# Optimization experiments

Hardware: AMD Instinct MI355X
Metric: run time of the kernel (lower is better)

## Reference

```python
import jax, jax.numpy as jnp
import numpy as np

EMBED_DIM = 1024
HEADS = 16
HEAD_DIM = EMBED_DIM // HEADS
N, SEQ = 2, 2048


def setup_inputs() -> dict:
    key = jax.random.key(0)
    ks = jax.random.split(key, 9)
    s = 1.0 / np.sqrt(HEAD_DIM)
    inp = {
        "values": jax.random.normal(ks[0], (N, SEQ, EMBED_DIM), jnp.float32),
        "keys": jax.random.normal(ks[1], (N, SEQ, EMBED_DIM), jnp.float32),
        "query": jax.random.normal(ks[2], (N, SEQ, EMBED_DIM), jnp.float32),
        "mask": jax.random.randint(ks[3], (N, 1, SEQ, SEQ), 0, 2, jnp.int32),
        # per-head projection weights (torch Linear: y = x @ W.T)
        "Wv": jax.random.normal(ks[4], (HEAD_DIM, HEAD_DIM), jnp.float32) * s,
        "Wk": jax.random.normal(ks[5], (HEAD_DIM, HEAD_DIM), jnp.float32) * s,
        "Wq": jax.random.normal(ks[6], (HEAD_DIM, HEAD_DIM), jnp.float32) * s,
        "Wo": jax.random.normal(ks[7], (EMBED_DIM, EMBED_DIM), jnp.float32) * (1.0 / np.sqrt(EMBED_DIM)),
        "bo": jax.random.normal(ks[8], (EMBED_DIM,), jnp.float32) * 0.01,
    }
    return inp


def reference(values, keys, query, mask, Wv, Wk, Wq, Wo, bo):
    n, q_len = query.shape[0], query.shape[1]
    v_len, k_len = values.shape[1], keys.shape[1]
    # reshape to [N, len, H, D]
    v = values.reshape(n, v_len, HEADS, HEAD_DIM)
    k = keys.reshape(n, k_len, HEADS, HEAD_DIM)
    q = query.reshape(n, q_len, HEADS, HEAD_DIM)
    # per-head linear projections (shared weight across heads), torch: x @ W.T
    v = jnp.einsum("nlhd,ed->nlhe", v, Wv)
    k = jnp.einsum("nlhd,ed->nlhe", k, Wk)
    q = jnp.einsum("nlhd,ed->nlhe", q, Wq)
    # energy: [N, H, Q, K]
    energy = jnp.einsum("nqhd,nkhd->nhqk", q, k)
    energy = jnp.where(mask == 0, jnp.float32(-1e20), energy)
    # NOTE: original scales by sqrt(embed_dim), not sqrt(head_dim)
    attention = jax.nn.softmax(energy / jnp.sqrt(jnp.float32(EMBED_DIM)), axis=3)
    out = jnp.einsum("nhql,nlhd->nqhd", attention, v).reshape(n, q_len, EMBED_DIM)
    out = out @ Wo.T + bo  # fc_out; dropout is identity in eval mode
    return out
```

## Files before the change

### kernel.cpp

```cpp
#include <hip/hip_runtime.h>
#include <hip/hip_bf16.h>

#define NB 2
#define SEQ 2048
#define HEADS 16
#define HD 64
#define ED 1024

typedef __bf16 bf16x8 __attribute__((ext_vector_type(8)));
typedef float f32x4 __attribute__((ext_vector_type(4)));
typedef unsigned short u16x8 __attribute__((ext_vector_type(8)));
typedef unsigned short u16x4 __attribute__((ext_vector_type(4)));

__device__ __forceinline__ unsigned short f2bf(float f) {
    unsigned u = __builtin_bit_cast(unsigned, f);
    u += 0x7fffu + ((u >> 16) & 1u);
    return (unsigned short)(u >> 16);
}

__device__ __forceinline__ bf16x8 cvt8(const float* __restrict__ p) {
    const float4* p4 = (const float4*)p;
    float4 a = p4[0], b = p4[1];
    u16x8 u;
    u[0] = f2bf(a.x); u[1] = f2bf(a.y); u[2] = f2bf(a.z); u[3] = f2bf(a.w);
    u[4] = f2bf(b.x); u[5] = f2bf(b.y); u[6] = f2bf(b.z); u[7] = f2bf(b.w);
    return __builtin_bit_cast(bf16x8, u);
}

__device__ __forceinline__ bf16x8 ldfrag(const void* p) {
    uint4 v = *(const uint4*)p;
    return __builtin_bit_cast(bf16x8, v);
}

__device__ __forceinline__ f32x4 mfma16(bf16x8 a, bf16x8 b, f32x4 c) {
    return __builtin_amdgcn_mfma_f32_16x16x32_bf16(a, b, c, 0, 0, 0);
}

__device__ __forceinline__ unsigned packbf(float lo, float hi) {
    unsigned a = __builtin_bit_cast(unsigned, hi) + 0x8000u;
    unsigned b = __builtin_bit_cast(unsigned, lo) + 0x8000u;
    return __builtin_amdgcn_perm(a, b, 0x07060302u);
}

#define GLOAD_LDS(gp, lp) \
    __builtin_amdgcn_global_load_lds( \
        (const __attribute__((address_space(1))) unsigned int*)(gp), \
        (__attribute__((address_space(3))) unsigned int*)(lp), 16, 0, 0)

#define QSCALE 0.04508422f

__global__ __launch_bounds__(256) void mask_bits_kernel(
    const int* __restrict__ mask, unsigned long long* __restrict__ bits)
{
    size_t i = (size_t)blockIdx.x * 256 + threadIdx.x;
    int m = mask[i];
    unsigned long long b = __ballot(m != 0);
    if ((threadIdx.x & 63) == 0) bits[i >> 6] = b;
}

__global__ __launch_bounds__(256) void wo_cvt_kernel(
    const float* __restrict__ Wo, unsigned short* __restrict__ Wob)
{
    size_t i = ((size_t)blockIdx.x * 256 + threadIdx.x) * 4;
    float4 v = *(const float4*)(Wo + i);
    u16x4 u;
    u[0] = f2bf(v.x); u[1] = f2bf(v.y); u[2] = f2bf(v.z); u[3] = f2bf(v.w);
    *(u16x4*)(Wob + i) = u;
}

__global__ __launch_bounds__(256) void proj_kernel(
    const float* __restrict__ qin, const float* __restrict__ kin, const float* __restrict__ vin,
    const float* __restrict__ Wq, const float* __restrict__ Wk, const float* __restrict__ Wv,
    unsigned short* __restrict__ Qb, unsigned short* __restrict__ Kb,
    unsigned short* __restrict__ Vt)
{
    __shared__ __align__(16) char tile[64 * 144];

    int t3  = blockIdx.x >> 10;
    int rem = blockIdx.x & 1023;
    int h   = rem >> 6;
    int rt  = rem & 63;
    int wave = threadIdx.x >> 6, lane = threadIdx.x & 63;
    int quad = lane >> 4, l16 = lane & 15;

    const float* in = (t3 == 0) ? qin : ((t3 == 1) ? kin : vin);
    const float* W  = (t3 == 0) ? Wq  : ((t3 == 1) ? Wk  : Wv);

    int r0 = rt * 64 + wave * 16;

    bf16x8 bf0[4], bf1[4];
#pragma unroll
    for (int sl = 0; sl < 4; ++sl) {
        const float* wrow = W + (sl * 16 + l16) * 64;
        bf0[sl] = cvt8(wrow + quad * 8);
        bf1[sl] = cvt8(wrow + 32 + quad * 8);
    }
    const float* xrow = in + (size_t)(r0 + l16) * ED + h * 64;
    bf16x8 af0 = cvt8(xrow + quad * 8);
    bf16x8 af1 = cvt8(xrow + 32 + quad * 8);

    f32x4 acc[4];
#pragma unroll
    for (int sl = 0; sl < 4; ++sl) {
        f32x4 c = {0.f, 0.f, 0.f, 0.f};
        c = mfma16(af0, bf0[sl], c);
        c = mfma16(af1, bf1[sl], c);
        acc[sl] = c;
    }
    float sc = (t3 == 0) ? QSCALE : 1.0f;

    size_t nh = (size_t)((r0 >> 11) * HEADS + h);
    int rl = lane >> 3, cl = lane & 7;

    if (t3 != 2) {
#pragma unroll
        for (int r = 0; r < 4; ++r) {
            int srow = wave * 16 + quad * 4 + r;
#pragma unroll
            for (int sl = 0; sl < 4; ++sl)
                *(unsigned short*)(tile + srow * 144 + (sl * 16 + l16) * 2) =
                    f2bf(acc[sl][r] * sc);
        }
        unsigned short* dst = (t3 == 0) ? Qb : Kb;
        int s0 = (r0 & 2047);
#pragma unroll
        for (int g = 0; g < 2; ++g) {
            int lrow = wave * 16 + g * 8 + rl;
            uint4 v = *(const uint4*)(tile + lrow * 144 + cl * 16);
            *(uint4*)(dst + (nh * SEQ + (s0 & ~15) + g * 8 + rl) * HD + cl * 8) = v;
        }
    } else {
#pragma unroll
        for (int r = 0; r < 4; ++r) {
            int srow = wave * 16 + quad * 4 + r;
#pragma unroll
            for (int sl = 0; sl < 4; ++sl)
                *(unsigned short*)(tile + (sl * 16 + l16) * 144 + srow * 2) =
                    f2bf(acc[sl][r]);
        }
        __syncthreads();
        int s_tile = rt & 31;
#pragma unroll
        for (int g = 0; g < 2; ++g) {
            int erow = wave * 16 + g * 8 + rl;
            uint4 v = *(const uint4*)(tile + erow * 144 + cl * 16);
            *(uint4*)(Vt + ((nh * 32 + s_tile) * 64 + erow) * 64 + cl * 8) = v;
        }
    }
}

template <int SPLIT>
__global__ __launch_bounds__(256, 4) void attn_kernel(
    const unsigned short* __restrict__ Qb, const unsigned short* __restrict__ Kb,
    const unsigned short* __restrict__ Vt2, const unsigned long long* __restrict__ mb,
    unsigned short* __restrict__ Ab, float* __restrict__ Of, float* __restrict__ Ls)
{
    __shared__ __align__(16) char smem[24576 + 4 * 2304];

    int tid = threadIdx.x;
    int wave = tid >> 6, lane = tid & 63;
    int quad = lane >> 4, l16 = lane & 15;

    int b   = blockIdx.x;
    int xcd = b & 7;
    int j   = b >> 3;
    int nh, qb, half;
    if (SPLIT) { nh = xcd * 4 + (j >> 5); int r = j & 31; qb = r >> 1; half = r & 1; }
    else       { nh = xcd * 4 + (j >> 4); qb = j & 15; half = 0; }
    int n = nh >> 4, h = nh & 15;
    int q0 = qb * 128 + wave * 32;

    size_t headoff = (size_t)nh * SEQ * HD;
    bf16x8 qf[2][2];
#pragma unroll
    for (int t = 0; t < 2; ++t) {
        const unsigned short* qrow = Qb + headoff + (size_t)(q0 + t * 16 + l16) * HD;
        qf[t][0] = ldfrag(qrow + quad * 8);
        qf[t][1] = ldfrag(qrow + 32 + quad * 8);
    }

    int srow = lane >> 3, sslot = lane & 7;
    int stoff = srow * 128 + (((sslot - srow) & 7) * 16);

    int rotA = ((quad + l16) & 7) * 16;
    int aK0 = l16 * 128 + rotA;
    int aV  = 16384 + l16 * 128 + rotA;
    int aVx = aV ^ 64;
    char* pbase = smem + 24576 + wave * 2304;
    char* pw = pbase + l16 * 144 + quad * 8;
    char* pr = pbase + l16 * 144 + quad * 16;

    const unsigned short* gK = Kb + headoff;
    const unsigned short* gV = Vt2 + (size_t)nh * (32 * 4096);
    const unsigned long long* mbase = mb + (size_t)n * (SEQ * SEQ / 64)
                                         + (size_t)(q0 + l16) * (SEQ / 64);

    u16x8 ou;
#pragma unroll
    for (int jj = 0; jj < 8; ++jj) ou[jj] = 0x3F80;
    bf16x8 ones = __builtin_bit_cast(bf16x8, ou);

    f32x4 o[2][4] = {{{0,0,0,0},{0,0,0,0},{0,0,0,0},{0,0,0,0}},
                     {{0,0,0,0},{0,0,0,0},{0,0,0,0},{0,0,0,0}}};
    f32x4 lacc[2] = {{0,0,0,0},{0,0,0,0}};
    int qsh = quad * 4;

    int kb0   = SPLIT ? half * (SEQ / 2) : 0;
    int kbend = SPLIT ? kb0 + (SEQ / 2) : SEQ;

    {
        const char* sK = (const char*)(gK + (size_t)kb0 * 64) + stoff;
        const char* sV = (const char*)(gV + (size_t)(kb0 >> 6) * 4096) + stoff;
#pragma unroll
        for (int i2 = 0; i2 < 2; ++i2) {
            int c = wave * 2 + i2;
            GLOAD_LDS(sK + c * 1024, smem + c * 1024);
            GLOAD_LDS(sV + c * 1024, smem + 16384 + c * 1024);
        }
    }

    int par = 0;
    for (int kb = kb0; kb < kbend; kb += 64) {
        int kbn = (kb + 64) & (SEQ - 1);
        __syncthreads();
        {
            const char* sK = (const char*)(gK + (size_t)kbn * 64) + stoff;
            char* dK = smem + (par ^ 1) * 8192;
#pragma unroll
            for (int i2 = 0; i2 < 2; ++i2) {
                int c = wave * 2 + i2;
                GLOAD_LDS(sK + c * 1024, dK + c * 1024);
            }
        }
        unsigned long long m64[2];
#pragma unroll
        for (int t = 0; t < 2; ++t)
            m64[t] = mbase[(size_t)(t * 16) * (SEQ / 64) + (kb >> 6)] >> qsh;

        const char* kbuf = smem + par * 8192;
        bf16x8 kf[4][2];
#pragma unroll
        for (int kt = 0; kt < 4; ++kt) {
            kf[kt][0] = ldfrag(kbuf + aK0 + kt * 2048);
            kf[kt][1] = ldfrag(kbuf + (aK0 ^ 64) + kt * 2048);
        }
#pragma unroll
        for (int t = 0; t < 2; ++t) {
            f32x4 c[4];
#pragma unroll
            for (int kt = 0; kt < 4; ++kt) {
                f32x4 cc = {0.f, 0.f, 0.f, 0.f};
                cc = mfma16(kf[kt][0], qf[t][0], cc);
                cc = mfma16(kf[kt][1], qf[t][1], cc);
                c[kt] = cc;
            }
            unsigned mlo = (unsigned)m64[t];
            unsigned mhi = (unsigned)(m64[t] >> 32);
#pragma unroll
            for (int kt = 0; kt < 4; ++kt) {
                unsigned mw = (kt & 2) ? mhi : mlo;
                int bs = (kt & 1) ? 16 : 0;
                float p0 = ((mw >> (bs + 0)) & 1u) ? __builtin_exp2f(c[kt][0]) : 0.f;
                float p1 = ((mw >> (bs + 1)) & 1u) ? __builtin_exp2f(c[kt][1]) : 0.f;
                float p2 = ((mw >> (bs + 2)) & 1u) ? __builtin_exp2f(c[kt][2]) : 0.f;
                float p3 = ((mw >> (bs + 3)) & 1u) ? __builtin_exp2f(c[kt][3]) : 0.f;
                uint2 dw = { packbf(p0, p1), packbf(p2, p3) };
                *(uint2*)(pw + kt * 32) = dw;
            }
            bf16x8 pb0 = ldfrag(pr);
            bf16x8 pb1 = ldfrag(pr + 64);
            lacc[t] = mfma16(ones, pb0, lacc[t]);
            lacc[t] = mfma16(ones, pb1, lacc[t]);
#pragma unroll
            for (int sl = 0; sl < 4; ++sl) {
                o[t][sl] = mfma16(ldfrag(smem + aV  + sl * 2048), pb0, o[t][sl]);
                o[t][sl] = mfma16(ldfrag(smem + aVx + sl * 2048), pb1, o[t][sl]);
            }
        }
        __syncthreads();
        {
            const char* sV = (const char*)(gV + (size_t)(kbn >> 6) * 4096) + stoff;
#pragma unroll
            for (int i2 = 0; i2 < 2; ++i2) {
                int c = wave * 2 + i2;
                GLOAD_LDS(sV + c * 1024, smem + 16384 + c * 1024);
            }
        }
        par ^= 1;
    }

#pragma unroll
    for (int t = 0; t < 2; ++t) {
        float s = lacc[t][0];
        int q = q0 + t * 16 + l16;
        if (SPLIT) {
            size_t qg = (size_t)nh * SEQ + q;
            if (quad == 0) Ls[(size_t)half * 65536 + qg] = s;
            float* op = Of + ((size_t)half * 65536 + qg) * 64 + qsh;
#pragma unroll
            for (int sl = 0; sl < 4; ++sl) {
                float4 v = { o[t][sl][0], o[t][sl][1], o[t][sl][2], o[t][sl][3] };
                *(float4*)(op + sl * 16) = v;
            }
        } else {
            float rinv = 1.0f / s;
            unsigned short* op = Ab + (((size_t)(n * SEQ + q)) * HEADS + h) * HD + qsh;
#pragma unroll
            for (int sl = 0; sl < 4; ++sl) {
                u16x4 u;
                u[0] = f2bf(o[t][sl][0] * rinv);
                u[1] = f2bf(o[t][sl][1] * rinv);
                u[2] = f2bf(o[t][sl][2] * rinv);
                u[3] = f2bf(o[t][sl][3] * rinv);
                *(u16x4*)(op + sl * 16) = u;
            }
        }
    }
}

__global__ __launch_bounds__(256) void combine_kernel(
    const float* __restrict__ Of, const float* __restrict__ Ls,
    unsigned short* __restrict__ Ab)
{
    int idx = blockIdx.x * 256 + threadIdx.x;
    int q  = idx >> 4;
    int d0 = (idx & 15) * 4;
    const float4 o0 = *(const float4*)(Of + (size_t)q * 64 + d0);
    const float4 o1 = *(const float4*)(Of + 4194304 + (size_t)q * 64 + d0);
    float rl = 1.0f / (Ls[q] + Ls[65536 + q]);
    int n = q >> 15, h = (q >> 11) & 15, s = q & 2047;
    size_t ab = (((size_t)(n * SEQ + s)) * HEADS + h) * HD + d0;
    u16x4 u;
    u[0] = f2bf((o0.x + o1.x) * rl);
    u[1] = f2bf((o0.y + o1.y) * rl);
    u[2] = f2bf((o0.z + o1.z) * rl);
    u[3] = f2bf((o0.w + o1.w) * rl);
    *(u16x4*)(Ab + ab) = u;
}

__global__ __launch_bounds__(256) void out_gemm_kernel(
    const unsigned short* __restrict__ Ab, const unsigned short* __restrict__ Wob,
    const float* __restrict__ bo, float* __restrict__ out)
{
    __shared__ __align__(16) char lds[32768];

    int wave = threadIdx.x >> 6, lane = threadIdx.x & 63;
    int quad = lane >> 4, l16 = lane & 15;
    int rt = blockIdx.x >> 3, ct = blockIdx.x & 7;
    int wr = wave >> 1, wc = wave & 1;

    int srow = lane >> 3, sslot = lane & 7;
    int stoff = srow * 2048 + (((sslot - srow) & 7) * 16);
    const char* gA = (const char*)Ab  + (size_t)rt * 128 * 2048 + stoff;
    const char* gB = (const char*)Wob + (size_t)ct * 128 * 2048 + stoff;

    int aA[4], aB[4];
#pragma unroll
    for (int i = 0; i < 4; ++i) {
        int rowA = wr * 64 + i * 16 + l16;
        aA[i] = rowA * 128 + (((quad + rowA) & 7) * 16);
        int rowB = wc * 64 + i * 16 + l16;
        aB[i] = 16384 + rowB * 128 + (((quad + rowB) & 7) * 16);
    }

    f32x4 acc[4][4] = {};
    for (int f = 0; f < ED; f += 64) {
        __syncthreads();
#pragma unroll
        for (int i = 0; i < 4; ++i) {
            int c = wave * 4 + i;
            GLOAD_LDS(gA + (size_t)c * 16384 + f * 2, lds + c * 1024);
            GLOAD_LDS(gB + (size_t)c * 16384 + f * 2, lds + 16384 + c * 1024);
        }
        __syncthreads();
#pragma unroll
        for (int kk = 0; kk < 2; ++kk) {
            int x = kk * 64;
            bf16x8 af[4], bfr[4];
#pragma unroll
            for (int i = 0; i < 4; ++i)  af[i]  = ldfrag(lds + (aA[i] ^ x));
#pragma unroll
            for (int sl = 0; sl < 4; ++sl) bfr[sl] = ldfrag(lds + (aB[sl] ^ x));
#pragma unroll
            for (int i = 0; i < 4; ++i)
#pragma unroll
                for (int sl = 0; sl < 4; ++sl)
                    acc[i][sl] = mfma16(af[i], bfr[sl], acc[i][sl]);
        }
    }

    float bv[4];
#pragma unroll
    for (int sl = 0; sl < 4; ++sl)
        bv[sl] = bo[ct * 128 + wc * 64 + sl * 16 + l16];
#pragma unroll
    for (int i = 0; i < 4; ++i)
#pragma unroll
        for (int r = 0; r < 4; ++r) {
            int row = rt * 128 + wr * 64 + i * 16 + quad * 4 + r;
#pragma unroll
            for (int sl = 0; sl < 4; ++sl) {
                int e = ct * 128 + wc * 64 + sl * 16 + l16;
                out[(size_t)row * ED + e] = acc[i][sl][r] + bv[sl];
            }
        }
}

extern "C" void kernel_launch(void* const* d_in, const int* in_sizes, int n_in,
                              void* d_out, int out_size, void* d_ws, size_t ws_size,
                              hipStream_t stream)
{
    const float* values = (const float*)d_in[0];
    const float* keys   = (const float*)d_in[1];
    const float* query  = (const float*)d_in[2];
    const int*   mask   = (const int*)d_in[3];
    const float* Wv     = (const float*)d_in[4];
    const float* Wk     = (const float*)d_in[5];
    const float* Wq     = (const float*)d_in[6];
    const float* Wo     = (const float*)d_in[7];
    const float* bo     = (const float*)d_in[8];
    float* out = (float*)d_out;

    char* w = (char*)d_ws;
    unsigned short* Qb  = (unsigned short*)(w);
    unsigned short* Kb  = (unsigned short*)(w +  8388608);
    unsigned short* Vt  = (unsigned short*)(w + 16777216);
    unsigned short* Ab  = (unsigned short*)(w + 25165824);
    unsigned long long* Mb = (unsigned long long*)(w + 33554432);
    unsigned short* Wob = (unsigned short*)(w + 34603008);
    float* Of = (float*)(w + 36700160);
    float* Ls = (float*)(w + 70254592);

    bool split = ws_size >= 70778880ULL;

    mask_bits_kernel<<<NB * SEQ * SEQ / 256, 256, 0, stream>>>(mask, Mb);
    wo_cvt_kernel<<<ED * ED / (256 * 4), 256, 0, stream>>>(Wo, Wob);
    proj_kernel<<<3 * HEADS * 64, 256, 0, stream>>>(query, keys, values, Wq, Wk, Wv, Qb, Kb, Vt);
    if (split) {
        attn_kernel<1><<<1024, 256, 0, stream>>>(Qb, Kb, Vt, Mb, Ab, Of, Ls);
        combine_kernel<<<4096, 256, 0, stream>>>(Of, Ls, Ab);
    } else {
        attn_kernel<0><<<512, 256, 0, stream>>>(Qb, Kb, Vt, Mb, Ab, Of, Ls);
    }
    out_gemm_kernel<<<256, 256, 0, stream>>>(Ab, Wob, bo, out);
}
```

Baseline: 252.6 us.

## Double-buffer output GEMM LDS, halve column tile, merge prep kernels

Merges the mask-bit packing and Wo bf16 conversion into one launch, saving a kernel launch. The output projection GEMM now uses 128x64 tiles instead of 128x128, doubling the grid to 512 blocks so more CUs have work. It also double-buffers the LDS loads so the next K-slice is fetched while the current one is multiplied, with one barrier per iteration. The cost is more LDS per block (48KB), lower arithmetic intensity per tile, and a wrapped prefetch on the last iteration that does redundant loads.

```diff
diff --git a/kernel.cpp b/kernel.cpp
--- a/kernel.cpp
+++ b/kernel.cpp
@@ -49,23 +49,23 @@
 
 #define QSCALE 0.04508422f
 
-__global__ __launch_bounds__(256) void mask_bits_kernel(
-    const int* __restrict__ mask, unsigned long long* __restrict__ bits)
-{
-    size_t i = (size_t)blockIdx.x * 256 + threadIdx.x;
-    int m = mask[i];
-    unsigned long long b = __ballot(m != 0);
-    if ((threadIdx.x & 63) == 0) bits[i >> 6] = b;
-}
-
-__global__ __launch_bounds__(256) void wo_cvt_kernel(
+__global__ __launch_bounds__(256) void prep_kernel(
+    const int* __restrict__ mask, unsigned long long* __restrict__ bits,
     const float* __restrict__ Wo, unsigned short* __restrict__ Wob)
 {
-    size_t i = ((size_t)blockIdx.x * 256 + threadIdx.x) * 4;
-    float4 v = *(const float4*)(Wo + i);
-    u16x4 u;
-    u[0] = f2bf(v.x); u[1] = f2bf(v.y); u[2] = f2bf(v.z); u[3] = f2bf(v.w);
-    *(u16x4*)(Wob + i) = u;
+    int bid = blockIdx.x;
+    if (bid < NB * SEQ * SEQ / 256) {
+        size_t i = (size_t)bid * 256 + threadIdx.x;
+        int m = mask[i];
+        unsigned long long b = __ballot(m != 0);
+        if ((threadIdx.x & 63) == 0) bits[i >> 6] = b;
+    } else {
+        size_t i = ((size_t)(bid - NB * SEQ * SEQ / 256) * 256 + threadIdx.x) * 4;
+        float4 v = *(const float4*)(Wo + i);
+        u16x4 u;
+        u[0] = f2bf(v.x); u[1] = f2bf(v.y); u[2] = f2bf(v.z); u[3] = f2bf(v.w);
+        *(u16x4*)(Wob + i) = u;
+    }
 }
 
 __global__ __launch_bounds__(256) void proj_kernel(
@@ -342,65 +342,92 @@
     const unsigned short* __restrict__ Ab, const unsigned short* __restrict__ Wob,
     const float* __restrict__ bo, float* __restrict__ out)
 {
-    __shared__ __align__(16) char lds[32768];
-
-    int wave = threadIdx.x >> 6, lane = threadIdx.x & 63;
+    __shared__ __align__(16) char lds[49152];
+
+    int tid = threadIdx.x;
+    int wave = tid >> 6, lane = tid & 63;
     int quad = lane >> 4, l16 = lane & 15;
-    int rt = blockIdx.x >> 3, ct = blockIdx.x & 7;
+    int rt = blockIdx.x >> 4, ct = blockIdx.x & 15;
     int wr = wave >> 1, wc = wave & 1;
 
     int srow = lane >> 3, sslot = lane & 7;
     int stoff = srow * 2048 + (((sslot - srow) & 7) * 16);
     const char* gA = (const char*)Ab  + (size_t)rt * 128 * 2048 + stoff;
-    const char* gB = (const char*)Wob + (size_t)ct * 128 * 2048 + stoff;
-
-    int aA[4], aB[4];
+    const char* gB = (const char*)Wob + (size_t)ct * 64 * 2048 + stoff;
+
+    int aA[4], aB[2];
 #pragma unroll
     for (int i = 0; i < 4; ++i) {
         int rowA = wr * 64 + i * 16 + l16;
         aA[i] = rowA * 128 + (((quad + rowA) & 7) * 16);
-        int rowB = wc * 64 + i * 16 + l16;
-        aB[i] = 16384 + rowB * 128 + (((quad + rowB) & 7) * 16);
-    }
-
-    f32x4 acc[4][4] = {};
+    }
+#pragma unroll
+    for (int sl = 0; sl < 2; ++sl) {
+        int rowB = wc * 32 + sl * 16 + l16;
+        aB[sl] = rowB * 128 + (((quad + rowB) & 7) * 16);
+    }
+
+#pragma unroll
+    for (int i = 0; i < 4; ++i) {
+        int c = wave * 4 + i;
+        GLOAD_LDS(gA + (size_t)c * 16384, lds + c * 1024);
+    }
+#pragma unroll
+    for (int i = 0; i < 2; ++i) {
+        int c = wave * 2 + i;
+        GLOAD_LDS(gB + (size_t)c * 16384, lds + 32768 + c * 1024);
+    }
+
+    f32x4 acc[4][2] = {};
+    int par = 0;
     for (int f = 0; f < ED; f += 64) {
+        int fn = (f + 64) & (ED - 1);
         __syncthreads();
-#pragma unroll
-        for (int i = 0; i < 4; ++i) {
-            int c = wave * 4 + i;
-            GLOAD_LDS(gA + (size_t)c * 16384 + f * 2, lds + c * 1024);
-            GLOAD_LDS(gB + (size_t)c * 16384 + f * 2, lds + 16384 + c * 1024);
-        }
-        __syncthreads();
+        {
+            int pA = (par ^ 1) * 16384;
+            int pB = 32768 + (par ^ 1) * 8192;
+#pragma unroll
+            for (int i = 0; i < 4; ++i) {
+                int c = wave * 4 + i;
+                GLOAD_LDS(gA + (size_t)c * 16384 + fn * 2, lds + pA + c * 1024);
+            }
+#pragma unroll
+            for (int i = 0; i < 2; ++i) {
+                int c = wave * 2 + i;
+                GLOAD_LDS(gB + (size_t)c * 16384 + fn * 2, lds + pB + c * 1024);
+            }
+        }
+        int bA = par * 16384;
+        int bB = 32768 + par * 8192;
 #pragma unroll
         for (int kk = 0; kk < 2; ++kk) {
             int x = kk * 64;
-            bf16x8 af[4], bfr[4];
-#pragma unroll
-            for (int i = 0; i < 4; ++i)  af[i]  = ldfrag(lds + (aA[i] ^ x));
-#pragma unroll
-            for (int sl = 0; sl < 4; ++sl) bfr[sl] = ldfrag(lds + (aB[sl] ^ x));
+            bf16x8 af[4], bfr[2];
+#pragma unroll
+            for (int i = 0; i < 4; ++i)    af[i]  = ldfrag(lds + bA + (aA[i] ^ x));
+#pragma unroll
+            for (int sl = 0; sl < 2; ++sl) bfr[sl] = ldfrag(lds + bB + (aB[sl] ^ x));
 #pragma unroll
             for (int i = 0; i < 4; ++i)
 #pragma unroll
-                for (int sl = 0; sl < 4; ++sl)
+                for (int sl = 0; sl < 2; ++sl)
                     acc[i][sl] = mfma16(af[i], bfr[sl], acc[i][sl]);
         }
-    }
-
-    float bv[4];
-#pragma unroll
-    for (int sl = 0; sl < 4; ++sl)
-        bv[sl] = bo[ct * 128 + wc * 64 + sl * 16 + l16];
+        par ^= 1;
+    }
+
+    float bv[2];
+#pragma unroll
+    for (int sl = 0; sl < 2; ++sl)
+        bv[sl] = bo[ct * 64 + wc * 32 + sl * 16 + l16];
 #pragma unroll
     for (int i = 0; i < 4; ++i)
 #pragma unroll
         for (int r = 0; r < 4; ++r) {
             int row = rt * 128 + wr * 64 + i * 16 + quad * 4 + r;
 #pragma unroll
-            for (int sl = 0; sl < 4; ++sl) {
-                int e = ct * 128 + wc * 64 + sl * 16 + l16;
+            for (int sl = 0; sl < 2; ++sl) {
+                int e = ct * 64 + wc * 32 + sl * 16 + l16;
                 out[(size_t)row * ED + e] = acc[i][sl][r] + bv[sl];
             }
         }
@@ -433,8 +460,7 @@
 
     bool split = ws_size >= 70778880ULL;
 
-    mask_bits_kernel<<<NB * SEQ * SEQ / 256, 256, 0, stream>>>(mask, Mb);
-    wo_cvt_kernel<<<ED * ED / (256 * 4), 256, 0, stream>>>(Wo, Wob);
+    prep_kernel<<<NB * SEQ * SEQ / 256 + ED * ED / 1024, 256, 0, stream>>>(mask, Mb, Wo, Wob);
     proj_kernel<<<3 * HEADS * 64, 256, 0, stream>>>(query, keys, values, Wq, Wk, Wv, Qb, Kb, Vt);
     if (split) {
         attn_kernel<1><<<1024, 256, 0, stream>>>(Qb, Kb, Vt, Mb, Ab, Of, Ls);
@@ -442,5 +468,5 @@
     } else {
         attn_kernel<0><<<512, 256, 0, stream>>>(Qb, Kb, Vt, Mb, Ab, Of, Ls);
     }
-    out_gemm_kernel<<<256, 256, 0, stream>>>(Ab, Wob, bo, out);
-}
+    out_gemm_kernel<<<512, 256, 0, stream>>>(Ab, Wob, bo, out);
+}
```

Measured after the change: 243.9 us. 3.4% less time.
